# Optimization experiments

Measured on AMD Instinct MI355X. Metric: run time of the kernel, lower is better.

Reference implementation:

```python
import jax, jax.numpy as jnp
import numpy as np
from jax import lax

B, H, W = 10, 320, 1024
PTS, DENSE, WD, KMEAN = 500, 2000, 11, 10
N = B * PTS  # 5000 center rows


def setup_inputs() -> dict:
    key = jax.random.key(0)
    k1, k2, k3, k4, k5, k6 = jax.random.split(key, 6)
    disp = jax.random.uniform(k1, (B, 1, H, W), dtype=jnp.float32)
    # forepred is a binary foreground prediction map -> strong Sobel edges
    forepred = jnp.round(jax.random.uniform(k2, (B, 1, H, W), dtype=jnp.float32))
    centerx = jax.random.randint(k3, (N,), WD, W - WD, dtype=jnp.int32)
    centery = jax.random.randint(k4, (N,), WD, H - WD, dtype=jnp.int32)
    bx = jax.random.randint(k5, (N, DENSE), -WD, WD + 1, dtype=jnp.int32)
    by = jax.random.randint(k6, (N, DENSE), -7, 8, dtype=jnp.int32)
    return {"disp": disp, "forepred": forepred, "centerx": centerx,
            "centery": centery, "bx": bx, "by": by}


def _mask_grad(disp, forepred):
    # Sobel-x conv, padding=1, no bias
    wx = jnp.array([[-1., 0., 1.], [-2., 0., 2.], [-1., 0., 1.]],
                   dtype=forepred.dtype)[None, None]  # [1,1,3,3]
    g = lax.conv_general_dilated(forepred, wx, (1, 1), 'SAME')
    mg = jnp.abs(g)
    # 3x3 max-pool, stride 1, padding 1 ("expand")
    mg = lax.reduce_window(mg, -jnp.inf, lax.max, (1, 1, 3, 3), (1, 1, 1, 1), 'SAME')
    mg = mg * (disp > 0.007).astype(mg.dtype)
    mg = jnp.maximum(mg, 3.0) - 3.0  # clamp(min=3) - 3
    # zero 4-pixel borders (zeroArea = [0,1,2,3,-1,-2,-3,-4])
    zy = jnp.array([0, 1, 2, 3, H - 1, H - 2, H - 3, H - 4])
    zx = jnp.array([0, 1, 2, 3, W - 1, W - 2, W - 3, W - 4])
    mg = mg.at[:, :, zy, :].set(0.0)
    mg = mg.at[:, :, :, zx].set(0.0)
    return mg


def reference(disp, forepred, centerx, centery, bx, by):
    maskGrad = _mask_grad(disp, forepred)
    channelInd = jnp.repeat(jnp.arange(B, dtype=jnp.int32), PTS)  # [N]
    # on-border row validity (original compacts; we mask instead, jit-friendly)
    validRow = maskGrad[channelInd, 0, centery, centerx] > 0.1  # [N]

    sampledx = centerx[:, None] + bx  # [N, DENSE]
    sampledy = centery[:, None] + by
    flat = (channelInd[:, None].astype(jnp.int32) * H + sampledy) * W + sampledx
    sampledDisp = disp.reshape(-1)[flat]  # irregular gather, [N, DENSE]

    kmeanLarge = jnp.max(sampledDisp, axis=1, keepdims=True)
    kmeanSmall = jnp.min(sampledDisp, axis=1, keepdims=True)
    for _ in range(KMEAN):
        distLarge = jnp.abs(sampledDisp - kmeanLarge)
        distSmall = jnp.abs(sampledDisp - kmeanSmall)
        belongingLarge = (distLarge <= distSmall).astype(sampledDisp.dtype)
        belongingSmall = 1.0 - belongingLarge
        kmeanLarge = (jnp.sum(sampledDisp * belongingLarge, axis=1, keepdims=True)
                      / jnp.sum(belongingLarge, axis=1, keepdims=True))
        kmeanSmall = (jnp.sum(sampledDisp * belongingSmall, axis=1, keepdims=True)
                      / jnp.sum(belongingSmall, axis=1, keepdims=True))

    contrast = ((kmeanLarge - kmeanSmall)[:, 0] > 0.005) & \
               (jnp.sum(belongingLarge, axis=1) > 5)
    keep = (validRow & contrast).astype(sampledDisp.dtype)  # [N]
    # per-row [large, small] cluster means; rows failing selection zeroed
    out = jnp.concatenate([kmeanLarge, kmeanSmall], axis=1) * keep[:, None]
    return out
```

## Files before the change

### kernel.cpp

```cpp
#include <hip/hip_runtime.h>

namespace {

constexpr int Bn    = 10;
constexpr int H     = 320;
constexpr int W     = 1024;
constexpr int PTS   = 500;
constexpr int DENSE = 2000;
constexpr int N     = Bn * PTS;
constexpr int HWp   = H * W;
constexpr int RPB   = 4;
constexpr int KITER = 10;

constexpr int WY   = 15;
constexpr int WX   = 24;
constexpr int WSZ  = WY * WX;
constexpr int WOFF = 7 * WX + 11;

__global__ __launch_bounds__(256, 6)
void rsbsp_kernel(const float* __restrict__ disp,
                  const float* __restrict__ forepred,
                  const int*   __restrict__ centerx,
                  const int*   __restrict__ centery,
                  const int*   __restrict__ bx,
                  const int*   __restrict__ by,
                  float*       __restrict__ out)
{
    __shared__ float win[RPB][WSZ];

    const int wid  = threadIdx.x >> 6;
    const int lane = threadIdx.x & 63;
    const int row  = blockIdx.x * RPB + wid;
    const int b    = row / PTS;
    const int cx   = centerx[row];
    const int cy   = centery[row];
    const float* db = disp     + b * HWp;
    const float* fb = forepred + b * HWp;

    float* wl = win[wid];
    const int gbase = (cy - 7) * W + (cx - 11);
    #pragma unroll
    for (int i = 0; i < 6; ++i) {
        const unsigned w = (unsigned)(lane + 64 * i);
        if (w < WSZ) {
            const unsigned r = w / 24u;
            const unsigned c = w - r * 24u;
            wl[w] = db[gbase + r * W + c];
        }
    }

    float F[5][5];
    #pragma unroll
    for (int a = 0; a < 5; ++a)
        #pragma unroll
        for (int c = 0; c < 5; ++c)
            F[a][c] = fb[(cy - 2 + a) * W + (cx - 2 + c)];

    float v = 0.f;
    #pragma unroll
    for (int dy = 0; dy < 3; ++dy)
        #pragma unroll
        for (int dx = 0; dx < 3; ++dx) {
            const float g = (F[dy    ][dx + 2] - F[dy    ][dx])
                    + 2.f * (F[dy + 1][dx + 2] - F[dy + 1][dx])
                    +       (F[dy + 2][dx + 2] - F[dy + 2][dx]);
            v = fmaxf(v, fabsf(g));
        }
    const float dcen = db[cy * W + cx];
    const float mgv  = fmaxf(v * ((dcen > 0.007f) ? 1.f : 0.f), 3.f) - 3.f;
    const bool validRow = mgv > 0.1f;

    const int4* bx4 = reinterpret_cast<const int4*>(bx + row * DENSE);
    const int4* by4 = reinterpret_cast<const int4*>(by + row * DENSE);

    float s[32];
    float mx = -INFINITY, mn = INFINITY, tot = 0.f;
    #pragma unroll
    for (int k = 0; k < 8; ++k) {
        const int q = lane + 64 * k;
        if (q < DENSE / 4) {
            const int4 xb = bx4[q];
            const int4 yb = by4[q];
            const float x0 = wl[yb.x * WX + xb.x + WOFF];
            const float x1 = wl[yb.y * WX + xb.y + WOFF];
            const float x2 = wl[yb.z * WX + xb.z + WOFF];
            const float x3 = wl[yb.w * WX + xb.w + WOFF];
            s[k * 4 + 0] = x0; s[k * 4 + 1] = x1;
            s[k * 4 + 2] = x2; s[k * 4 + 3] = x3;
            mx = fmaxf(fmaxf(fmaxf(mx, x0), fmaxf(x1, x2)), x3);
            mn = fminf(fminf(fminf(mn, x0), fminf(x1, x2)), x3);
            tot += (x0 + x1) + (x2 + x3);
        } else {
            s[k * 4 + 0] = -INFINITY; s[k * 4 + 1] = -INFINITY;
            s[k * 4 + 2] = -INFINITY; s[k * 4 + 3] = -INFINITY;
        }
    }

    #pragma unroll
    for (int m = 1; m < 64; m <<= 1) {
        mx  = fmaxf(mx, __shfl_xor(mx, m));
        mn  = fminf(mn, __shfl_xor(mn, m));
        tot += __shfl_xor(tot, m);
    }

    float mL = mx, mS = mn;
    int cntLast = 0;
    for (int it = 0; it < KITER; ++it) {
        const float mid = 0.5f * (mL + mS);
        float sumL = 0.f;
        int   cnt  = 0;
        #pragma unroll
        for (int j = 0; j < 32; ++j) {
            const float x  = s[j];
            const bool  bl = x >= mid;
            sumL += bl ? x : 0.f;
            cnt  += (int)__popcll(__ballot(bl));
        }
        #pragma unroll
        for (int m = 1; m < 64; m <<= 1) sumL += __shfl_xor(sumL, m);

        const float cf = (float)cnt;
        const float df = (float)DENSE - cf;
        if (it < KITER - 1) {
            mL = sumL * __builtin_amdgcn_rcpf(cf);
            mS = (tot - sumL) * __builtin_amdgcn_rcpf(df);
        } else {
            mL = sumL / cf;
            mS = (tot - sumL) / df;
        }
        if (cnt == DENSE) mS = __int_as_float(0x7fc00000);
        cntLast = cnt;
    }

    if (lane == 0) {
        const bool contrast = ((mL - mS) > 0.005f) && (cntLast > 5);
        const float keep = (validRow && contrast) ? 1.f : 0.f;
        out[row * 2 + 0] = mL * keep;
        out[row * 2 + 1] = mS * keep;
    }
}

}

extern "C" void kernel_launch(void* const* d_in, const int* in_sizes, int n_in,
                              void* d_out, int out_size, void* d_ws, size_t ws_size,
                              hipStream_t stream) {
    const float* disp = (const float*)d_in[0];
    const float* fore = (const float*)d_in[1];
    const int*   cx   = (const int*)d_in[2];
    const int*   cy   = (const int*)d_in[3];
    const int*   bxp  = (const int*)d_in[4];
    const int*   byp  = (const int*)d_in[5];
    float* out = (float*)d_out;

    rsbsp_kernel<<<N / RPB, 256, 0, stream>>>(disp, fore, cx, cy, bxp, byp, out);
}
```

Before: 136.3 us.

## Assign one block per row, skip invalid rows, exit k-means early on convergence

Each 256-thread block now handles a single center row instead of one wavefront per row. The Sobel check is spread across threads through LDS, and rows that fail the border test exit before any bx/by loads or k-means work. The k-means loop combines per-wave partial sums through shared memory with a barrier each iteration, and it stops early once the count and sum stop changing. This cuts per-thread register use and skips work on invalid rows, but it adds block-wide synchronisation on every iteration and launches four times as many blocks.

```diff
diff --git a/kernel.cpp b/kernel.cpp
--- a/kernel.cpp
+++ b/kernel.cpp
@@ -9,7 +9,6 @@
 constexpr int DENSE = 2000;
 constexpr int N     = Bn * PTS;
 constexpr int HWp   = H * W;
-constexpr int RPB   = 4;
 constexpr int KITER = 10;
 
 constexpr int WY   = 15;
@@ -17,7 +16,7 @@
 constexpr int WSZ  = WY * WX;
 constexpr int WOFF = 7 * WX + 11;
 
-__global__ __launch_bounds__(256, 6)
+__global__ __launch_bounds__(256, 8)
 void rsbsp_kernel(const float* __restrict__ disp,
                   const float* __restrict__ forepred,
                   const int*   __restrict__ centerx,
@@ -26,65 +25,80 @@
                   const int*   __restrict__ by,
                   float*       __restrict__ out)
 {
-    __shared__ float win[RPB][WSZ];
+    __shared__ float ldsF[25];
+    __shared__ float ldsG[9];
+    __shared__ float win[WSZ];
+    __shared__ float cmb0[4][3];
+    __shared__ float cmb[2][4][2];
 
-    const int wid  = threadIdx.x >> 6;
-    const int lane = threadIdx.x & 63;
-    const int row  = blockIdx.x * RPB + wid;
-    const int b    = row / PTS;
-    const int cx   = centerx[row];
-    const int cy   = centery[row];
+    const int t   = threadIdx.x;
+    const int wid = t >> 6;
+    const int row = blockIdx.x;
+    const int b   = row / PTS;
+    const int cx  = centerx[row];
+    const int cy  = centery[row];
     const float* db = disp     + b * HWp;
     const float* fb = forepred + b * HWp;
 
-    float* wl = win[wid];
+    const float dcen = db[cy * W + cx];
+
+    float fpix = 0.f;
+    if (t < 25) {
+        const int r = t / 5, c = t % 5;
+        fpix = fb[(cy - 2 + r) * W + (cx - 2 + c)];
+    }
     const int gbase = (cy - 7) * W + (cx - 11);
-    #pragma unroll
-    for (int i = 0; i < 6; ++i) {
-        const unsigned w = (unsigned)(lane + 64 * i);
-        if (w < WSZ) {
-            const unsigned r = w / 24u;
-            const unsigned c = w - r * 24u;
-            wl[w] = db[gbase + r * W + c];
+    float w0, w1 = 0.f;
+    {
+        const unsigned r0 = (unsigned)t / 24u, c0 = (unsigned)t - r0 * 24u;
+        w0 = db[gbase + r0 * W + c0];
+        const int i1 = t + 256;
+        if (i1 < WSZ) {
+            const unsigned r1 = (unsigned)i1 / 24u, c1 = (unsigned)i1 - r1 * 24u;
+            w1 = db[gbase + r1 * W + c1];
         }
     }
+    if (t < 25) ldsF[t] = fpix;
+    win[t] = w0;
+    if (t + 256 < WSZ) win[t + 256] = w1;
+    __syncthreads();
 
-    float F[5][5];
-    #pragma unroll
-    for (int a = 0; a < 5; ++a)
-        #pragma unroll
-        for (int c = 0; c < 5; ++c)
-            F[a][c] = fb[(cy - 2 + a) * W + (cx - 2 + c)];
+    if (t < 9) {
+        const int dy = t / 3, dx = t % 3;
+        const float g =
+                  (ldsF[(dy    ) * 5 + dx + 2] - ldsF[(dy    ) * 5 + dx])
+           + 2.f * (ldsF[(dy + 1) * 5 + dx + 2] - ldsF[(dy + 1) * 5 + dx])
+           +       (ldsF[(dy + 2) * 5 + dx + 2] - ldsF[(dy + 2) * 5 + dx]);
+        ldsG[t] = fabsf(g);
+    }
+    __syncthreads();
 
     float v = 0.f;
     #pragma unroll
-    for (int dy = 0; dy < 3; ++dy)
-        #pragma unroll
-        for (int dx = 0; dx < 3; ++dx) {
-            const float g = (F[dy    ][dx + 2] - F[dy    ][dx])
-                    + 2.f * (F[dy + 1][dx + 2] - F[dy + 1][dx])
-                    +       (F[dy + 2][dx + 2] - F[dy + 2][dx]);
-            v = fmaxf(v, fabsf(g));
-        }
-    const float dcen = db[cy * W + cx];
-    const float mgv  = fmaxf(v * ((dcen > 0.007f) ? 1.f : 0.f), 3.f) - 3.f;
+    for (int j = 0; j < 9; ++j) v = fmaxf(v, ldsG[j]);
+    const float mgv = fmaxf(v * ((dcen > 0.007f) ? 1.f : 0.f), 3.f) - 3.f;
     const bool validRow = mgv > 0.1f;
+
+    if (!validRow) {
+        if (t == 0) { out[row * 2 + 0] = 0.f; out[row * 2 + 1] = 0.f; }
+        return;
+    }
 
     const int4* bx4 = reinterpret_cast<const int4*>(bx + row * DENSE);
     const int4* by4 = reinterpret_cast<const int4*>(by + row * DENSE);
 
-    float s[32];
+    float s[8];
     float mx = -INFINITY, mn = INFINITY, tot = 0.f;
     #pragma unroll
-    for (int k = 0; k < 8; ++k) {
-        const int q = lane + 64 * k;
+    for (int k = 0; k < 2; ++k) {
+        const int q = t + 256 * k;
         if (q < DENSE / 4) {
             const int4 xb = bx4[q];
             const int4 yb = by4[q];
-            const float x0 = wl[yb.x * WX + xb.x + WOFF];
-            const float x1 = wl[yb.y * WX + xb.y + WOFF];
-            const float x2 = wl[yb.z * WX + xb.z + WOFF];
-            const float x3 = wl[yb.w * WX + xb.w + WOFF];
+            const float x0 = win[yb.x * WX + xb.x + WOFF];
+            const float x1 = win[yb.y * WX + xb.y + WOFF];
+            const float x2 = win[yb.z * WX + xb.z + WOFF];
+            const float x3 = win[yb.w * WX + xb.w + WOFF];
             s[k * 4 + 0] = x0; s[k * 4 + 1] = x1;
             s[k * 4 + 2] = x2; s[k * 4 + 3] = x3;
             mx = fmaxf(fmaxf(fmaxf(mx, x0), fmaxf(x1, x2)), x3);
@@ -102,39 +116,53 @@
         mn  = fminf(mn, __shfl_xor(mn, m));
         tot += __shfl_xor(tot, m);
     }
+    if ((t & 63) == 0) { cmb0[wid][0] = mx; cmb0[wid][1] = mn; cmb0[wid][2] = tot; }
+    __syncthreads();
+    mx  = fmaxf(fmaxf(cmb0[0][0], cmb0[1][0]), fmaxf(cmb0[2][0], cmb0[3][0]));
+    mn  = fminf(fminf(cmb0[0][1], cmb0[1][1]), fminf(cmb0[2][1], cmb0[3][1]));
+    tot = (cmb0[0][2] + cmb0[1][2]) + (cmb0[2][2] + cmb0[3][2]);
 
     float mL = mx, mS = mn;
-    int cntLast = 0;
+    float cntLast = 0.f;
+    float prevSum = -1.f, prevCnt = -1.f;
+    #pragma unroll 1
     for (int it = 0; it < KITER; ++it) {
         const float mid = 0.5f * (mL + mS);
         float sumL = 0.f;
-        int   cnt  = 0;
+        int   cw   = 0;
         #pragma unroll
-        for (int j = 0; j < 32; ++j) {
+        for (int j = 0; j < 8; ++j) {
             const float x  = s[j];
             const bool  bl = x >= mid;
             sumL += bl ? x : 0.f;
-            cnt  += (int)__popcll(__ballot(bl));
+            cw   += (int)__popcll(__ballot(bl));
         }
         #pragma unroll
         for (int m = 1; m < 64; m <<= 1) sumL += __shfl_xor(sumL, m);
 
-        const float cf = (float)cnt;
+        const int par = it & 1;
+        if ((t & 63) == 0) { cmb[par][wid][0] = sumL; cmb[par][wid][1] = (float)cw; }
+        __syncthreads();
+        sumL = (cmb[par][0][0] + cmb[par][1][0]) + (cmb[par][2][0] + cmb[par][3][0]);
+        const float cf = (cmb[par][0][1] + cmb[par][1][1]) + (cmb[par][2][1] + cmb[par][3][1]);
         const float df = (float)DENSE - cf;
-        if (it < KITER - 1) {
-            mL = sumL * __builtin_amdgcn_rcpf(cf);
-            mS = (tot - sumL) * __builtin_amdgcn_rcpf(df);
-        } else {
+
+        const bool done = (it == KITER - 1) || (cf == prevCnt && sumL == prevSum);
+        if (done) {
             mL = sumL / cf;
             mS = (tot - sumL) / df;
+            if (cf == (float)DENSE) mS = __int_as_float(0x7fc00000);
+            cntLast = cf;
+            break;
         }
-        if (cnt == DENSE) mS = __int_as_float(0x7fc00000);
-        cntLast = cnt;
+        mL = sumL * __builtin_amdgcn_rcpf(cf);
+        mS = (tot - sumL) * __builtin_amdgcn_rcpf(df);
+        prevSum = sumL; prevCnt = cf;
     }
 
-    if (lane == 0) {
-        const bool contrast = ((mL - mS) > 0.005f) && (cntLast > 5);
-        const float keep = (validRow && contrast) ? 1.f : 0.f;
+    if (t == 0) {
+        const bool contrast = ((mL - mS) > 0.005f) && (cntLast > 5.f);
+        const float keep = contrast ? 1.f : 0.f;
         out[row * 2 + 0] = mL * keep;
         out[row * 2 + 1] = mS * keep;
     }
@@ -153,5 +181,5 @@
     const int*   byp  = (const int*)d_in[5];
     float* out = (float*)d_out;
 
-    rsbsp_kernel<<<N / RPB, 256, 0, stream>>>(disp, fore, cx, cy, bxp, byp, out);
+    rsbsp_kernel<<<N, 256, 0, stream>>>(disp, fore, cx, cy, bxp, byp, out);
 }
```

Result: faster. 125.4 us (-8.0%).

## Early-exit invalid rows, spread Sobel over lanes, stop k-means at convergence

Applied to the files above, without the earlier changes.

The per-row Sobel/maxpool validity test is now computed first, with 9 lanes each evaluating one Sobel tap and a shuffle max-reduction. Rows that fail the test write zeros and return before the disparity window load and the bx/by gather. The k-means loop stops early once the cluster sum and count repeat, and the occupancy hint drops from 6 to 4. This skips gather and iteration work for rejected or converged rows, at the cost of wave divergence within blocks and a slight change in which reciprocal is used on the final iteration.

```diff
diff --git a/kernel.cpp b/kernel.cpp
--- a/kernel.cpp
+++ b/kernel.cpp
@@ -9,15 +9,15 @@
 constexpr int DENSE = 2000;
 constexpr int N     = Bn * PTS;
 constexpr int HWp   = H * W;
+constexpr int KITER = 10;
 constexpr int RPB   = 4;
-constexpr int KITER = 10;
 
 constexpr int WY   = 15;
 constexpr int WX   = 24;
 constexpr int WSZ  = WY * WX;
 constexpr int WOFF = 7 * WX + 11;
 
-__global__ __launch_bounds__(256, 6)
+__global__ __launch_bounds__(256, 4)
 void rsbsp_kernel(const float* __restrict__ disp,
                   const float* __restrict__ forepred,
                   const int*   __restrict__ centerx,
@@ -37,38 +37,39 @@
     const float* db = disp     + b * HWp;
     const float* fb = forepred + b * HWp;
 
+    float v = 0.f;
+    if (lane < 9) {
+        const int dy = lane / 3, dx = lane % 3;
+        const float* fp = fb + (cy - 2 + dy) * W + (cx - 2 + dx);
+        const float g = (fp[2]         - fp[0])
+                + 2.f * (fp[W + 2]     - fp[W])
+                +       (fp[2 * W + 2] - fp[2 * W]);
+        v = fabsf(g);
+    }
+    #pragma unroll
+    for (int m = 1; m < 16; m <<= 1) v = fmaxf(v, __shfl_xor(v, m));
+    v = __shfl(v, 0, 64);
+
+    const float dcen = db[cy * W + cx];
+    const float mgv  = fmaxf(v * ((dcen > 0.007f) ? 1.f : 0.f), 3.f) - 3.f;
+    const bool validRow = mgv > 0.1f;
+
+    if (!validRow) {
+        if (lane == 0) { out[row * 2 + 0] = 0.f; out[row * 2 + 1] = 0.f; }
+        return;
+    }
+
     float* wl = win[wid];
     const int gbase = (cy - 7) * W + (cx - 11);
     #pragma unroll
     for (int i = 0; i < 6; ++i) {
-        const unsigned w = (unsigned)(lane + 64 * i);
+        const int w = lane + 64 * i;
         if (w < WSZ) {
-            const unsigned r = w / 24u;
-            const unsigned c = w - r * 24u;
+            const unsigned r = (unsigned)w / 24u;
+            const unsigned c = (unsigned)w - r * 24u;
             wl[w] = db[gbase + r * W + c];
         }
     }
-
-    float F[5][5];
-    #pragma unroll
-    for (int a = 0; a < 5; ++a)
-        #pragma unroll
-        for (int c = 0; c < 5; ++c)
-            F[a][c] = fb[(cy - 2 + a) * W + (cx - 2 + c)];
-
-    float v = 0.f;
-    #pragma unroll
-    for (int dy = 0; dy < 3; ++dy)
-        #pragma unroll
-        for (int dx = 0; dx < 3; ++dx) {
-            const float g = (F[dy    ][dx + 2] - F[dy    ][dx])
-                    + 2.f * (F[dy + 1][dx + 2] - F[dy + 1][dx])
-                    +       (F[dy + 2][dx + 2] - F[dy + 2][dx]);
-            v = fmaxf(v, fabsf(g));
-        }
-    const float dcen = db[cy * W + cx];
-    const float mgv  = fmaxf(v * ((dcen > 0.007f) ? 1.f : 0.f), 3.f) - 3.f;
-    const bool validRow = mgv > 0.1f;
 
     const int4* bx4 = reinterpret_cast<const int4*>(bx + row * DENSE);
     const int4* by4 = reinterpret_cast<const int4*>(by + row * DENSE);
@@ -104,37 +105,41 @@
     }
 
     float mL = mx, mS = mn;
-    int cntLast = 0;
+    float cntLast = 0.f;
+    float prevSum = -1.f, prevCnt = -1.f;
+    #pragma unroll 1
     for (int it = 0; it < KITER; ++it) {
         const float mid = 0.5f * (mL + mS);
         float sumL = 0.f;
-        int   cnt  = 0;
+        int   cw   = 0;
         #pragma unroll
         for (int j = 0; j < 32; ++j) {
             const float x  = s[j];
             const bool  bl = x >= mid;
             sumL += bl ? x : 0.f;
-            cnt  += (int)__popcll(__ballot(bl));
+            cw   += (int)__popcll(__ballot(bl));
         }
         #pragma unroll
         for (int m = 1; m < 64; m <<= 1) sumL += __shfl_xor(sumL, m);
 
-        const float cf = (float)cnt;
+        const float cf = (float)cw;
         const float df = (float)DENSE - cf;
-        if (it < KITER - 1) {
-            mL = sumL * __builtin_amdgcn_rcpf(cf);
-            mS = (tot - sumL) * __builtin_amdgcn_rcpf(df);
-        } else {
+        const bool done = (it == KITER - 1) || (cf == prevCnt && sumL == prevSum);
+        if (done) {
             mL = sumL / cf;
             mS = (tot - sumL) / df;
+            if (cw == DENSE) mS = __int_as_float(0x7fc00000);
+            cntLast = cf;
+            break;
         }
-        if (cnt == DENSE) mS = __int_as_float(0x7fc00000);
-        cntLast = cnt;
+        mL = sumL * __builtin_amdgcn_rcpf(cf);
+        mS = (tot - sumL) * __builtin_amdgcn_rcpf(df);
+        prevSum = sumL; prevCnt = cf;
     }
 
     if (lane == 0) {
-        const bool contrast = ((mL - mS) > 0.005f) && (cntLast > 5);
-        const float keep = (validRow && contrast) ? 1.f : 0.f;
+        const bool contrast = ((mL - mS) > 0.005f) && (cntLast > 5.f);
+        const float keep = contrast ? 1.f : 0.f;
         out[row * 2 + 0] = mL * keep;
         out[row * 2 + 1] = mS * keep;
     }
```

Result: faster. 125.6 us (-7.8%).
